# Kernel tuning notes

Measured on AMD Instinct MI355X. Metric: run time of the kernel, lower is better.

Reference implementation:

```python
import math
import jax, jax.numpy as jnp
import numpy as np
from jax import lax

# dimensions
B_, H_, W_, w_ = 2, 28, 28, 7
L_ = H_ * W_
DM, EXPAND = 384, 2
DIN = DM * EXPAND            # 768
DS, DCONV = 16, 4
DTR = math.ceil(DM / 16)     # 24
HG, WG = H_ // w_, W_ // w_
K_ = 4                       # directions: h, v, w7, w7_flip

# ---- MultiScan scan/reverse permutations ----
def scan_h(x):  # [B,L,C] -> [B,C,L]
    return jnp.swapaxes(x, 1, 2)

def scan_v(x):  # 'b (h w) d -> b d (w h)'
    B, L, C = x.shape
    return x.reshape(B, H_, W_, C).transpose(0, 3, 2, 1).reshape(B, C, L)

def scan_w(x, flip):  # local windowed scan, w=7
    B, L, C = x.shape
    x = x.reshape(B, HG, w_, WG, w_, C).transpose(0, 5, 1, 3, 2, 4).reshape(B, C, L)
    return x[:, :, ::-1] if flip else x

def rev_h(x):  # [B,C,L] -> [B,C,L]
    return x

def rev_v(x):  # 'b d (h w) -> b d (w h)'
    B, C, L = x.shape
    return x.reshape(B, C, H_, W_).transpose(0, 1, 3, 2).reshape(B, C, L)

def rev_w(x, flip):
    B, C, L = x.shape
    if flip:
        x = x[:, :, ::-1]
    return x.reshape(B, C, HG, WG, w_, w_).transpose(0, 1, 2, 4, 3, 5).reshape(B, C, L)

# ---- mamba_inner (causal depthwise conv + silu + selective scan) ----
def mamba_inner(xz, conv_w, conv_b, x_proj_w, dt_w, dt_b, A_log, Dp):
    # xz: [B, 2*DIN, L]
    B = xz.shape[0]
    x, z = xz[:, :DIN], xz[:, DIN:]
    xpad = jnp.pad(x, ((0, 0), (0, 0), (DCONV - 1, 0)))  # causal padding
    conv = lax.conv_general_dilated(
        xpad, conv_w[:, None, :], (1,), 'VALID',
        dimension_numbers=('NCH', 'OIH', 'NCH'), feature_group_count=DIN)
    conv = conv + conv_b[None, :, None]
    conv = conv * jax.nn.sigmoid(conv)  # silu
    x_dbl = jnp.einsum('bdl,ed->bel', conv, x_proj_w)  # [B, DTR+2*DS, L]
    dt, Bm, Cm = x_dbl[:, :DTR], x_dbl[:, DTR:DTR + DS], x_dbl[:, DTR + DS:]
    delta = jax.nn.softplus(jnp.einsum('brl,dr->bdl', dt, dt_w) + dt_b[None, :, None])
    A = -jnp.exp(A_log)  # [DIN, DS]
    dA = jnp.exp(jnp.einsum('bdl,dn->lbdn', delta, A))      # [L,B,DIN,DS]
    dBu = jnp.einsum('bdl,bnl,bdl->lbdn', delta, Bm, conv)  # [L,B,DIN,DS]
    Ct = jnp.moveaxis(Cm, -1, 0)                            # [L,B,DS]
    def step(h, inp):
        a, bu, c = inp
        h = a * h + bu
        return h, jnp.einsum('bdn,bn->bd', h, c)
    h0 = jnp.zeros((B, DIN, DS), xz.dtype)
    _, ys = lax.scan(step, h0, (dA, dBu, Ct))  # ys: [L,B,DIN]
    y = jnp.moveaxis(ys, 0, -1) + Dp[:, None] * conv
    return y * (z * jax.nn.sigmoid(z))  # gated with silu(z)

# ---- BiAttn channel gating (shared params across directions) ----
def biattn(x, ln_g, ln_b, gr_w, gr_b, cs_w, cs_b):
    # x: [..., L, DIN]
    mu = x.mean(-1, keepdims=True)
    var = x.var(-1, keepdims=True)
    xn = (x - mu) * lax.rsqrt(var + 1e-5) * ln_g + ln_b
    g = xn.mean(-2, keepdims=True)  # global token
    g = jax.nn.gelu(g @ gr_w.T + gr_b, approximate=False)
    attn = jax.nn.sigmoid(g @ cs_w.T + cs_b)
    return x * attn

def _forward(x, in_proj_w, conv_w, conv_b, x_proj_w, dt_w, dt_b, A_log, Dp,
             ln_g, ln_b, gr_w, gr_b, cs_w, cs_b, out_proj_w):
    xz = x @ in_proj_w.T  # [B,L,2*DIN]
    xs = jnp.stack([scan_h(xz), scan_v(xz), scan_w(xz, False), scan_w(xz, True)])  # [K,B,2DIN,L]
    ys = jax.vmap(mamba_inner)(xs, conv_w, conv_b, x_proj_w, dt_w, dt_b, A_log, Dp)  # [K,B,DIN,L]
    outs = jnp.stack([rev_h(ys[0]), rev_v(ys[1]), rev_w(ys[2], False), rev_w(ys[3], True)])
    outs = jnp.swapaxes(outs, -2, -1)  # [K,B,L,DIN]
    outs = biattn(outs, ln_g, ln_b, gr_w, gr_b, cs_w, cs_b)
    out = outs.sum(0)  # MultiScan merge (search=False)
    return out @ out_proj_w.T  # [B,L,DM]

def setup_inputs() -> dict:
    key = jax.random.key(0)
    ks = jax.random.split(key, 10)
    f = jnp.float32
    return {
        'x': jax.random.normal(ks[0], (B_, L_, DM), f),
        'in_proj_w': jax.random.normal(ks[1], (2 * DIN, DM), f) * 0.02,
        'conv_w': jax.random.normal(ks[2], (K_, DIN, DCONV), f) * 0.2,
        'conv_b': jax.random.normal(ks[3], (K_, DIN), f) * 0.02,
        'x_proj_w': jax.random.normal(ks[4], (K_, DTR + 2 * DS, DIN), f) * 0.02,
        'dt_w': jax.random.normal(ks[5], (K_, DIN, DTR), f) * 0.02,
        'dt_b': jax.random.normal(ks[6], (K_, DIN), f) * 0.02 - 4.0,
        'A_log': jnp.log(jnp.tile(jnp.arange(1, DS + 1, dtype=f)[None, None], (K_, DIN, 1))),
        'Dp': jnp.ones((K_, DIN), f),
        'ln_g': jnp.ones((DIN,), f),
        'ln_b': jnp.zeros((DIN,), f),
        'gr_w': jax.random.normal(ks[7], (DIN // 8, DIN), f) * 0.02,
        'gr_b': jnp.zeros((DIN // 8,), f),
        'cs_w': jax.random.normal(ks[8], (DIN, DIN // 8), f) * 0.02,
        'cs_b': jnp.zeros((DIN,), f),
        'out_proj_w': jax.random.normal(ks[9], (DM, DIN), f) * 0.02,
    }

def reference(x, in_proj_w, conv_w, conv_b, x_proj_w, dt_w, dt_b, A_log, Dp,
              ln_g, ln_b, gr_w, gr_b, cs_w, cs_b, out_proj_w):
    return _forward(x, in_proj_w, conv_w, conv_b, x_proj_w, dt_w, dt_b, A_log, Dp,
                    ln_g, ln_b, gr_w, gr_b, cs_w, cs_b, out_proj_w)
```

## Files before the change

### kernel.cpp

```cpp
#include <hip/hip_runtime.h>
#include <math.h>

#define Bb 2
#define Hh 28
#define Ww 28
#define Ll 784
#define DMm 384
#define DINn 768
#define DSs 16
#define DTRr 24
#define Ee 56
#define Kk 4
#define BL 1568
#define NC 56
#define CH 14

typedef short s8v __attribute__((ext_vector_type(8)));
typedef float f4v __attribute__((ext_vector_type(4)));

__device__ __forceinline__ unsigned short f2bf(float f) {
    unsigned int u = __float_as_uint(f);
    return (unsigned short)((u + 0x7fffu + ((u >> 16) & 1u)) >> 16);
}
__device__ __forceinline__ float bf2f(unsigned short s) {
    return __uint_as_float(((unsigned int)s) << 16);
}

__device__ __forceinline__ int spos(int k, int l) {
    if (k == 0) return l;
    if (k == 1) return (l % 28) * 28 + l / 28;
    if (k == 3) l = 783 - l;
    int j = l % 7;
    int i = (l / 7) % 7;
    int wg = (l / 49) % 4;
    int hg = l / 196;
    return (hg * 7 + i) * 28 + wg * 7 + j;
}


__global__ __launch_bounds__(256) void gemm_mfma(
    const float* __restrict__ A, const float* __restrict__ B, float* __restrict__ Cc,
    int M, int N, int K, int lda, int ldb, int ldc,
    long sA, long sB, long sC, int nsk)
{
    int zz = blockIdx.z;
    int sk = zz % nsk, z = zz / nsk;
    int Kc = K / nsk;
    const float* Ab = A + (long)z * sA + (long)sk * Kc;
    const float* Bp = B + (long)z * sB + (long)sk * Kc;
    float* Cb = Cc + (long)zz * sC;

    __shared__ __align__(16) short Ah[64][40];
    __shared__ __align__(16) short Al[64][40];
    __shared__ __align__(16) short Bh[64][40];
    __shared__ __align__(16) short Bl[64][40];

    int t = threadIdx.x;
    int m0 = blockIdx.y * 64, n0 = blockIdx.x * 64;
    int srow = t >> 2, skq = t & 3;
    int am = m0 + srow;
    int bn = n0 + srow;
    int w = t >> 6, lane = t & 63;
    int wr = (w >> 1) * 32, wc = (w & 1) * 32;
    int lr = lane & 15, lg = lane >> 4;

    f4v acc[2][2] = {};

    int nsteps = Kc / 32;
    float4 a0, a1, b0, b1;
    {
        int koff = skq * 8;
        if (am < M) { a0 = *(const float4*)(Ab + (long)am * lda + koff);
                      a1 = *(const float4*)(Ab + (long)am * lda + koff + 4); }
        else        { a0 = make_float4(0.f,0.f,0.f,0.f); a1 = a0; }
        if (bn < N) { b0 = *(const float4*)(Bp + (long)bn * ldb + koff);
                      b1 = *(const float4*)(Bp + (long)bn * ldb + koff + 4); }
        else        { b0 = make_float4(0.f,0.f,0.f,0.f); b1 = b0; }
    }

    for (int it = 0; it < nsteps; ++it) {
        {
            float va[8] = {a0.x,a0.y,a0.z,a0.w,a1.x,a1.y,a1.z,a1.w};
            float vb[8] = {b0.x,b0.y,b0.z,b0.w,b1.x,b1.y,b1.z,b1.w};
            s8v ah, al2, bh, bl2;
#pragma unroll
            for (int j = 0; j < 8; ++j) {
                unsigned short h = f2bf(va[j]);
                ah[j]  = (short)h;
                al2[j] = (short)f2bf(va[j] - bf2f(h));
                unsigned short g = f2bf(vb[j]);
                bh[j]  = (short)g;
                bl2[j] = (short)f2bf(vb[j] - bf2f(g));
            }
            *(s8v*)&Ah[srow][skq * 8] = ah;
            *(s8v*)&Al[srow][skq * 8] = al2;
            *(s8v*)&Bh[srow][skq * 8] = bh;
            *(s8v*)&Bl[srow][skq * 8] = bl2;
        }
        __syncthreads();

        float4 na0, na1, nb0, nb1;
        if (it + 1 < nsteps) {
            int koff = (it + 1) * 32 + skq * 8;
            if (am < M) { na0 = *(const float4*)(Ab + (long)am * lda + koff);
                          na1 = *(const float4*)(Ab + (long)am * lda + koff + 4); }
            else        { na0 = make_float4(0.f,0.f,0.f,0.f); na1 = na0; }
            if (bn < N) { nb0 = *(const float4*)(Bp + (long)bn * ldb + koff);
                          nb1 = *(const float4*)(Bp + (long)bn * ldb + koff + 4); }
            else        { nb0 = make_float4(0.f,0.f,0.f,0.f); nb1 = nb0; }
        }

        s8v fah[2], fal[2], fbh[2], fbl[2];
#pragma unroll
        for (int rb = 0; rb < 2; ++rb) {
            int r = wr + rb * 16 + lr;
            fah[rb] = *(const s8v*)&Ah[r][lg * 8];
            fal[rb] = *(const s8v*)&Al[r][lg * 8];
        }
#pragma unroll
        for (int cb = 0; cb < 2; ++cb) {
            int c = wc + cb * 16 + lr;
            fbh[cb] = *(const s8v*)&Bh[c][lg * 8];
            fbl[cb] = *(const s8v*)&Bl[c][lg * 8];
        }
#pragma unroll
        for (int rb = 0; rb < 2; ++rb)
#pragma unroll
            for (int cb = 0; cb < 2; ++cb) {
                acc[rb][cb] = __builtin_amdgcn_mfma_f32_16x16x32_bf16(fah[rb], fbh[cb], acc[rb][cb], 0, 0, 0);
                acc[rb][cb] = __builtin_amdgcn_mfma_f32_16x16x32_bf16(fah[rb], fbl[cb], acc[rb][cb], 0, 0, 0);
                acc[rb][cb] = __builtin_amdgcn_mfma_f32_16x16x32_bf16(fal[rb], fbh[cb], acc[rb][cb], 0, 0, 0);
            }
        __syncthreads();
        a0 = na0; a1 = na1; b0 = nb0; b1 = nb1;
    }

#pragma unroll
    for (int rb = 0; rb < 2; ++rb)
#pragma unroll
        for (int cb = 0; cb < 2; ++cb) {
            int n = n0 + wc + cb * 16 + lr;
            if (n >= N) continue;
#pragma unroll
            for (int j = 0; j < 4; ++j) {
                int m = m0 + wr + rb * 16 + lg * 4 + j;
                if (m < M) Cb[(long)m * ldc + n] = acc[rb][cb][j];
            }
        }
}

__global__ __launch_bounds__(256) void reduce_sk(
    const float* __restrict__ part, float* __restrict__ out,
    int M, int Nv, int ldp, int ldo, int nsk, long sSlice, long sOutZ, int nz)
{
    long idx = (long)blockIdx.x * 256 + threadIdx.x;
    long tot = (long)nz * M * Nv;
    if (idx >= tot) return;
    int n = (int)(idx % Nv);
    long r = idx / Nv;
    int m = (int)(r % M);
    int z = (int)(r / M);
    float s = 0.f;
    for (int sk = 0; sk < nsk; ++sk)
        s += part[(long)(z * nsk + sk) * sSlice + (long)m * ldp + n];
    out[(long)z * sOutZ + (long)m * ldo + n] = s;
}

__global__ __launch_bounds__(256) void wsum_kernel(
    const float* __restrict__ outy, const float* __restrict__ attn,
    float* __restrict__ sbuf)
{
    long idx4 = (long)blockIdx.x * 256 + threadIdx.x;
    long tot4 = (long)Bb * Ll * DINn / 4;
    if (idx4 >= tot4) return;
    int d4 = (int)(idx4 % (DINn / 4));
    long bl = idx4 / (DINn / 4);
    int b = (int)(bl / Ll);
    int p = (int)(bl % Ll);
    float4 acc = make_float4(0.f, 0.f, 0.f, 0.f);
#pragma unroll
    for (int k = 0; k < Kk; ++k) {
        int kb = k * 2 + b;
        float4 y = reinterpret_cast<const float4*>(outy + ((long)kb * Ll + p) * DINn)[d4];
        float4 a = reinterpret_cast<const float4*>(attn + (long)kb * DINn)[d4];
        acc.x += y.x * a.x; acc.y += y.y * a.y;
        acc.z += y.z * a.z; acc.w += y.w * a.w;
    }
    reinterpret_cast<float4*>(sbuf)[idx4] = acc;
}

__global__ __launch_bounds__(256) void conv_kernel(
    const float* __restrict__ xz, const float* __restrict__ conv_w,
    const float* __restrict__ conv_b, float* __restrict__ conv,
    const float* __restrict__ dt_w, float* __restrict__ dtw_t)
{
    int l = blockIdx.x;
    int kb = blockIdx.y;
    int k = kb >> 1, b = kb & 1;
    if (kb == 0 && blockIdx.x < 12) {
        int t2 = blockIdx.x * 256 + threadIdx.x;
        int d2 = t2 % DINn, k2 = t2 / DINn;
#pragma unroll
        for (int r = 0; r < DTRr; ++r)
            dtw_t[((long)(k2 * DTRr + r)) * DINn + d2] = dt_w[((long)(k2 * DINn + d2)) * DTRr + r];
    }
    int p[4];
#pragma unroll
    for (int j = 0; j < 4; ++j) {
        int lp = l - 3 + j;
        p[j] = (lp >= 0) ? spos(k, lp) : -1;
    }
    for (int d = threadIdx.x; d < DINn; d += 256) {
        float acc = conv_b[k * DINn + d];
        const float* w = conv_w + (long)(k * DINn + d) * 4;
#pragma unroll
        for (int j = 0; j < 4; ++j) {
            if (p[j] >= 0)
                acc += w[j] * xz[((long)b * Ll + p[j]) * (2 * DINn) + d];
        }
        acc = acc / (1.f + __expf(-acc));
        conv[((long)kb * Ll + l) * DINn + d] = acc;
    }
}

__global__ __launch_bounds__(256) void scan1_kernel(
    const float* __restrict__ conv, const float* __restrict__ part3,
    const float* __restrict__ dtw_t, const float* __restrict__ dt_b,
    const float* __restrict__ Dp,
    float* __restrict__ outy, float* __restrict__ chunkB, float* __restrict__ chunkS,
    float* __restrict__ xdbl)
{
    int d = blockIdx.x * 256 + threadIdx.x;
    int c = blockIdx.y;
    int kb = blockIdx.z;
    int k = kb >> 1, b = kb & 1;

    __shared__ __align__(16) float xrow[CH][Ee];
    {
        int mbase = b * Ll + c * CH;
        for (int u = threadIdx.x; u < CH * Ee; u += 256) {
            int i = u / Ee, j = u % Ee;
            long base = ((long)(k * 8) * BL + mbase + i) * 56 + j;
            float s = 0.f;
#pragma unroll
            for (int sk = 0; sk < 8; ++sk)
                s += part3[base + (long)sk * BL * 56];
            xrow[i][j] = s;
            if (blockIdx.x == 0)
                xdbl[((long)kb * Ll + c * CH) * Ee + u] = s;
        }
    }
    __syncthreads();

    float dtw[DTRr];
#pragma unroll
    for (int r = 0; r < DTRr; ++r) dtw[r] = dtw_t[((long)(k * DTRr + r)) * DINn + d];
    float dtb = dt_b[k * DINn + d];
    float Dv = Dp[k * DINn + d];
    float h[DSs];
#pragma unroll
    for (int n = 0; n < DSs; ++n) h[n] = 0.f;

    const float* cl = conv + ((long)kb * Ll + c * CH) * DINn + d;
    float sumde = 0.f;
    for (int i = 0; i < CH; ++i) {
        const float4* xr = reinterpret_cast<const float4*>(&xrow[i][0]);
        float xlin = dtb;
#pragma unroll
        for (int g = 0; g < 6; ++g) {
            float4 q = xr[g];
            xlin += dtw[4*g] * q.x + dtw[4*g+1] * q.y + dtw[4*g+2] * q.z + dtw[4*g+3] * q.w;
        }
        float tE = __expf(xlin);
        float E = __builtin_amdgcn_rcpf(1.f + tE);
        float de = (xlin > 15.f) ? xlin : -__logf(E);
        float cv = cl[(long)i * DINn];
        sumde += de;
        float dexc = de * cv;
        float dAn = E;
        float y = Dv * cv;
#pragma unroll
        for (int g = 0; g < 4; ++g) {
            float4 Bq = xr[6 + g];
            float4 Cq = xr[10 + g];
            h[4*g+0] = dAn * h[4*g+0] + dexc * Bq.x; y += h[4*g+0] * Cq.x; dAn *= E;
            h[4*g+1] = dAn * h[4*g+1] + dexc * Bq.y; y += h[4*g+1] * Cq.y; dAn *= E;
            h[4*g+2] = dAn * h[4*g+2] + dexc * Bq.z; y += h[4*g+2] * Cq.z; dAn *= E;
            h[4*g+3] = dAn * h[4*g+3] + dexc * Bq.w; y += h[4*g+3] * Cq.w; dAn *= E;
        }
        int l = c * CH + i;
        int p = spos(k, l);
        outy[((long)kb * Ll + p) * DINn + d] = y;
    }
    long o = (long)(kb * NC + c);
    chunkS[o * DINn + d] = sumde;
#pragma unroll
    for (int n = 0; n < DSs; ++n)
        chunkB[(o * DSs + n) * DINn + d] = h[n];
}

__global__ __launch_bounds__(256) void scanfix_kernel(
    const float* __restrict__ chunkS, float* chunkB)
{
    int u = blockIdx.x * 256 + threadIdx.x;
    int d = u % DINn;
    int rest = u / DINn;
    int n = rest & 15;
    int kb = rest >> 4;
    float np1 = (float)(n + 1);
    float h = 0.f;
#pragma unroll
    for (int c = 0; c < NC; ++c) {
        long o = (long)(kb * NC + c);
        float S = chunkS[o * DINn + d];
        float a = __expf(-np1 * S);
        long idx = (o * DSs + n) * DINn + d;
        float bv = chunkB[idx];
        chunkB[idx] = h;
        h = a * h + bv;
    }
}

__global__ __launch_bounds__(768) void scan3_kernel(
    const float* __restrict__ xdbl, const float* __restrict__ dtw_t,
    const float* __restrict__ dt_b, const float* __restrict__ hin,
    const float* __restrict__ xz, float* __restrict__ outy,
    float* __restrict__ gpart)
{
    int d = threadIdx.x;
    int c = blockIdx.x;
    int kb = blockIdx.y;
    int k = kb >> 1, b = kb & 1;

    __shared__ __align__(16) float xrow[CH][Ee];
    {
        const float* src = xdbl + ((long)kb * Ll + c * CH) * Ee;
        for (int u = threadIdx.x; u < CH * Ee; u += 768)
            xrow[u / Ee][u % Ee] = src[u];
    }
    __syncthreads();

    float dtw[DTRr];
#pragma unroll
    for (int r = 0; r < DTRr; ++r) dtw[r] = dtw_t[((long)(k * DTRr + r)) * DINn + d];
    float dtb = dt_b[k * DINn + d];
    long o = (long)(kb * NC + c);
    float hc[DSs];
#pragma unroll
    for (int n = 0; n < DSs; ++n) hc[n] = hin[(o * DSs + n) * DINn + d];

    float v[CH];
    for (int i = 0; i < CH; ++i) {
        const float4* xr = reinterpret_cast<const float4*>(&xrow[i][0]);
        float xlin = dtb;
#pragma unroll
        for (int g = 0; g < 6; ++g) {
            float4 q = xr[g];
            xlin += dtw[4*g] * q.x + dtw[4*g+1] * q.y + dtw[4*g+2] * q.z + dtw[4*g+3] * q.w;
        }
        float E = __builtin_amdgcn_rcpf(1.f + __expf(xlin));
        int l = c * CH + i;
        int p = spos(k, l);
        long oy = ((long)kb * Ll + p) * DINn + d;
        float y = outy[oy];
        const float4* Cq4 = reinterpret_cast<const float4*>(&xrow[i][40]);
        float dAn = E;
#pragma unroll
        for (int g = 0; g < 4; ++g) {
            float4 Cq = Cq4[g];
            hc[4*g+0] *= dAn; y += hc[4*g+0] * Cq.x; dAn *= E;
            hc[4*g+1] *= dAn; y += hc[4*g+1] * Cq.y; dAn *= E;
            hc[4*g+2] *= dAn; y += hc[4*g+2] * Cq.z; dAn *= E;
            hc[4*g+3] *= dAn; y += hc[4*g+3] * Cq.w; dAn *= E;
        }
        float zv = xz[((long)b * Ll + p) * (2 * DINn) + DINn + d];
        y *= zv / (1.f + __expf(-zv));
        outy[oy] = y;
        v[i] = y;
    }

    int w = threadIdx.x >> 6, lane = threadIdx.x & 63;
    __shared__ float ps[12][CH], pss[12][CH];
    __shared__ float smu[CH], srs[CH];
#pragma unroll
    for (int i = 0; i < CH; ++i) {
        float s = v[i], ss = v[i] * v[i];
#pragma unroll
        for (int of = 32; of > 0; of >>= 1) {
            s += __shfl_down(s, of);
            ss += __shfl_down(ss, of);
        }
        if (lane == 0) { ps[w][i] = s; pss[w][i] = ss; }
    }
    __syncthreads();
    if (threadIdx.x < CH) {
        float s = 0.f, ss = 0.f;
#pragma unroll
        for (int w2 = 0; w2 < 12; ++w2) { s += ps[w2][threadIdx.x]; ss += pss[w2][threadIdx.x]; }
        float m = s / DINn;
        float var = ss / DINn - m * m;
        smu[threadIdx.x] = m;
        srs[threadIdx.x] = rsqrtf(var + 1e-5f);
    }
    __syncthreads();
    float acc = 0.f;
#pragma unroll
    for (int i = 0; i < CH; ++i) acc += (v[i] - smu[i]) * srs[i];
    gpart[(o) * DINn + d] = acc;
}

__global__ __launch_bounds__(768) void attn_kernel(
    const float* __restrict__ gpart, const float* __restrict__ ln_g,
    const float* __restrict__ ln_b, const float* __restrict__ gr_w,
    const float* __restrict__ gr_b, const float* __restrict__ cs_w,
    const float* __restrict__ cs_b, float* __restrict__ attn)
{
    __shared__ float gs[DINn];
    __shared__ float hs[96];
    int kb = blockIdx.x;
    int t = threadIdx.x;
    int w = t >> 6, lane = t & 63;
    {
        float s = 0.f;
#pragma unroll
        for (int c = 0; c < NC; ++c)
            s += gpart[((long)kb * NC + c) * DINn + t];
        gs[t] = ln_g[t] * (s / (float)Ll) + ln_b[t];
    }
    __syncthreads();
#pragma unroll
    for (int rr = 0; rr < 8; ++rr) {
        int r = w * 8 + rr;
        const float* wrow = gr_w + (long)r * DINn;
        float s = 0.f;
#pragma unroll
        for (int e = 0; e < 12; ++e) s += wrow[lane + 64 * e] * gs[lane + 64 * e];
#pragma unroll
        for (int o = 32; o > 0; o >>= 1) s += __shfl_down(s, o);
        if (lane == 0) {
            float a = s + gr_b[r];
            hs[r] = 0.5f * a * (1.f + erff(a * 0.70710678118654752f));
        }
    }
    __syncthreads();
    {
        float a = cs_b[t];
        const float4* wr = reinterpret_cast<const float4*>(cs_w + (long)t * 96);
#pragma unroll
        for (int e = 0; e < 24; ++e) {
            float4 q = wr[e];
            a += q.x * hs[4*e] + q.y * hs[4*e+1] + q.z * hs[4*e+2] + q.w * hs[4*e+3];
        }
        attn[kb * DINn + t] = 1.f / (1.f + __expf(-a));
    }
}

extern "C" void kernel_launch(void* const* d_in, const int* in_sizes, int n_in,
                              void* d_out, int out_size, void* d_ws, size_t ws_size,
                              hipStream_t stream) {
    const float* x         = (const float*)d_in[0];
    const float* in_proj_w = (const float*)d_in[1];
    const float* conv_w    = (const float*)d_in[2];
    const float* conv_b    = (const float*)d_in[3];
    const float* x_proj_w  = (const float*)d_in[4];
    const float* dt_w      = (const float*)d_in[5];
    const float* dt_b      = (const float*)d_in[6];
    const float* Dp        = (const float*)d_in[8];
    const float* ln_g      = (const float*)d_in[9];
    const float* ln_b      = (const float*)d_in[10];
    const float* gr_w      = (const float*)d_in[11];
    const float* gr_b      = (const float*)d_in[12];
    const float* cs_w      = (const float*)d_in[13];
    const float* cs_b      = (const float*)d_in[14];
    const float* out_proj_w= (const float*)d_in[15];
    float* out = (float*)d_out;

    float* ws     = (float*)d_ws;
    float* xz     = ws;
    float* conv   = xz    + (long)Bb * Ll * 2 * DINn;
    float* outy   = conv  + (long)Kk * BL * DINn;
    float* gpart  = outy  + (long)Kk * BL * DINn;
    float* attn   = gpart + (long)Kk * Bb * NC * DINn;
    float* dtw_t  = attn  + 2 * Kk * DINn;
    float* xdbl   = dtw_t + (long)Kk * DTRr * DINn;
    float* chunkB = xdbl  + (long)Kk * BL * Ee;
    float* chunkS = chunkB + (long)Kk * Bb * NC * DSs * DINn;
    float* part3  = chunkS + (long)Kk * Bb * NC * DINn;
    float* sbuf   = part3 + (long)32 * BL * 56;
    float* part10 = part3;

    gemm_mfma<<<dim3(1536 / 64, (BL + 63) / 64, 1), 256, 0, stream>>>(
        x, in_proj_w, xz, BL, 2 * DINn, DMm, DMm, DMm, 2 * DINn, 0, 0, 0, 1);

    conv_kernel<<<dim3(Ll, Kk * Bb), 256, 0, stream>>>(
        xz, conv_w, conv_b, conv, dt_w, dtw_t);

    gemm_mfma<<<dim3(1, (BL + 63) / 64, Kk * 8), 256, 0, stream>>>(
        conv, x_proj_w, part3, BL, Ee, DINn, DINn, DINn, 56,
        (long)BL * DINn, (long)Ee * DINn, (long)BL * 56, 8);

    scan1_kernel<<<dim3(DINn / 256, NC, Kk * Bb), 256, 0, stream>>>(
        conv, part3, dtw_t, dt_b, Dp, outy, chunkB, chunkS, xdbl);

    scanfix_kernel<<<dim3((Kk * Bb * DSs * DINn) / 256), 256, 0, stream>>>(
        chunkS, chunkB);

    scan3_kernel<<<dim3(NC, Kk * Bb), 768, 0, stream>>>(
        xdbl, dtw_t, dt_b, chunkB, xz, outy, gpart);

    attn_kernel<<<dim3(Kk * Bb), 768, 0, stream>>>(
        gpart, ln_g, ln_b, gr_w, gr_b, cs_w, cs_b, attn);

    wsum_kernel<<<dim3((Bb * Ll * DINn / 4 + 255) / 256), 256, 0, stream>>>(
        outy, attn, sbuf);

    gemm_mfma<<<dim3(DMm / 64, (BL + 63) / 64, 4), 256, 0, stream>>>(
        sbuf, out_proj_w, part10, BL, DMm, DINn, DINn, DINn, DMm,
        0, 0, (long)BL * DMm, 4);
    reduce_sk<<<dim3((BL * DMm + 255) / 256), 256, 0, stream>>>(
        part10, out, BL, DMm, DMm, DMm, 4, (long)BL * DMm, 0, 1);
}
```

Baseline: 258.4 us.

## Fuse attention into scan3 via last-block counter, atomic split-K output, wider scan1 blocks

Removes the separate attn_kernel by having the last-arriving scan3 block for each (k,b) compute the gated attention, using a global atomic counter with threadfences. The counter is reset in conv_kernel. The out_proj split-K GEMM now accumulates into the output with atomicAdd, after wsum zeroes it, which drops the reduce_sk kernel. scan1 is relaunched as one 768-thread block per chunk so each block covers all channels. Together these cut two kernel launches, but float atomics make summation order nondeterministic and the last-block pattern adds serialized tail work.

```diff
diff --git a/kernel.cpp b/kernel.cpp
--- a/kernel.cpp
+++ b/kernel.cpp
@@ -41,7 +41,7 @@
 __global__ __launch_bounds__(256) void gemm_mfma(
     const float* __restrict__ A, const float* __restrict__ B, float* __restrict__ Cc,
     int M, int N, int K, int lda, int ldb, int ldc,
-    long sA, long sB, long sC, int nsk)
+    long sA, long sB, long sC, int nsk, int atomic_out)
 {
     int zz = blockIdx.z;
     int sk = zz % nsk, z = zz / nsk;
@@ -144,33 +144,21 @@
 #pragma unroll
             for (int j = 0; j < 4; ++j) {
                 int m = m0 + wr + rb * 16 + lg * 4 + j;
-                if (m < M) Cb[(long)m * ldc + n] = acc[rb][cb][j];
+                if (m < M) {
+                    if (atomic_out) atomicAdd(&Cb[(long)m * ldc + n], acc[rb][cb][j]);
+                    else            Cb[(long)m * ldc + n] = acc[rb][cb][j];
+                }
             }
         }
-}
-
-__global__ __launch_bounds__(256) void reduce_sk(
-    const float* __restrict__ part, float* __restrict__ out,
-    int M, int Nv, int ldp, int ldo, int nsk, long sSlice, long sOutZ, int nz)
-{
-    long idx = (long)blockIdx.x * 256 + threadIdx.x;
-    long tot = (long)nz * M * Nv;
-    if (idx >= tot) return;
-    int n = (int)(idx % Nv);
-    long r = idx / Nv;
-    int m = (int)(r % M);
-    int z = (int)(r / M);
-    float s = 0.f;
-    for (int sk = 0; sk < nsk; ++sk)
-        s += part[(long)(z * nsk + sk) * sSlice + (long)m * ldp + n];
-    out[(long)z * sOutZ + (long)m * ldo + n] = s;
 }
 
 __global__ __launch_bounds__(256) void wsum_kernel(
     const float* __restrict__ outy, const float* __restrict__ attn,
-    float* __restrict__ sbuf)
+    float* __restrict__ sbuf, float* __restrict__ out)
 {
     long idx4 = (long)blockIdx.x * 256 + threadIdx.x;
+    if (idx4 < (long)BL * DMm / 4)
+        reinterpret_cast<float4*>(out)[idx4] = make_float4(0.f, 0.f, 0.f, 0.f);
     long tot4 = (long)Bb * Ll * DINn / 4;
     if (idx4 >= tot4) return;
     int d4 = (int)(idx4 % (DINn / 4));
@@ -192,11 +180,13 @@
 __global__ __launch_bounds__(256) void conv_kernel(
     const float* __restrict__ xz, const float* __restrict__ conv_w,
     const float* __restrict__ conv_b, float* __restrict__ conv,
-    const float* __restrict__ dt_w, float* __restrict__ dtw_t)
+    const float* __restrict__ dt_w, float* __restrict__ dtw_t,
+    int* __restrict__ ctr)
 {
     int l = blockIdx.x;
     int kb = blockIdx.y;
     int k = kb >> 1, b = kb & 1;
+    if (kb == 0 && blockIdx.x == 0 && threadIdx.x < 8) ctr[threadIdx.x] = 0;
     if (kb == 0 && blockIdx.x < 12) {
         int t2 = blockIdx.x * 256 + threadIdx.x;
         int d2 = t2 % DINn, k2 = t2 / DINn;
@@ -223,22 +213,22 @@
     }
 }
 
-__global__ __launch_bounds__(256) void scan1_kernel(
+__global__ __launch_bounds__(768) void scan1_kernel(
     const float* __restrict__ conv, const float* __restrict__ part3,
     const float* __restrict__ dtw_t, const float* __restrict__ dt_b,
     const float* __restrict__ Dp,
     float* __restrict__ outy, float* __restrict__ chunkB, float* __restrict__ chunkS,
     float* __restrict__ xdbl)
 {
-    int d = blockIdx.x * 256 + threadIdx.x;
-    int c = blockIdx.y;
-    int kb = blockIdx.z;
+    int d = threadIdx.x;
+    int c = blockIdx.x;
+    int kb = blockIdx.y;
     int k = kb >> 1, b = kb & 1;
 
     __shared__ __align__(16) float xrow[CH][Ee];
     {
         int mbase = b * Ll + c * CH;
-        for (int u = threadIdx.x; u < CH * Ee; u += 256) {
+        for (int u = threadIdx.x; u < CH * Ee; u += 768) {
             int i = u / Ee, j = u % Ee;
             long base = ((long)(k * 8) * BL + mbase + i) * 56 + j;
             float s = 0.f;
@@ -246,8 +236,7 @@
             for (int sk = 0; sk < 8; ++sk)
                 s += part3[base + (long)sk * BL * 56];
             xrow[i][j] = s;
-            if (blockIdx.x == 0)
-                xdbl[((long)kb * Ll + c * CH) * Ee + u] = s;
+            xdbl[((long)kb * Ll + c * CH) * Ee + u] = s;
         }
     }
     __syncthreads();
@@ -325,7 +314,11 @@
     const float* __restrict__ xdbl, const float* __restrict__ dtw_t,
     const float* __restrict__ dt_b, const float* __restrict__ hin,
     const float* __restrict__ xz, float* __restrict__ outy,
-    float* __restrict__ gpart)
+    float* __restrict__ gpart,
+    const float* __restrict__ ln_g, const float* __restrict__ ln_b,
+    const float* __restrict__ gr_w, const float* __restrict__ gr_b,
+    const float* __restrict__ cs_w, const float* __restrict__ cs_b,
+    float* __restrict__ attn, int* __restrict__ ctr)
 {
     int d = threadIdx.x;
     int c = blockIdx.x;
@@ -407,24 +400,22 @@
 #pragma unroll
     for (int i = 0; i < CH; ++i) acc += (v[i] - smu[i]) * srs[i];
     gpart[(o) * DINn + d] = acc;
-}
-
-__global__ __launch_bounds__(768) void attn_kernel(
-    const float* __restrict__ gpart, const float* __restrict__ ln_g,
-    const float* __restrict__ ln_b, const float* __restrict__ gr_w,
-    const float* __restrict__ gr_b, const float* __restrict__ cs_w,
-    const float* __restrict__ cs_b, float* __restrict__ attn)
-{
+
+    __threadfence();
+    __shared__ int lastf;
+    if (threadIdx.x == 0) lastf = (atomicAdd(&ctr[kb], 1) == NC - 1) ? 1 : 0;
+    __syncthreads();
+    if (!lastf) return;
+    __threadfence();
+
     __shared__ float gs[DINn];
     __shared__ float hs[96];
-    int kb = blockIdx.x;
     int t = threadIdx.x;
-    int w = t >> 6, lane = t & 63;
     {
         float s = 0.f;
 #pragma unroll
-        for (int c = 0; c < NC; ++c)
-            s += gpart[((long)kb * NC + c) * DINn + t];
+        for (int cc = 0; cc < NC; ++cc)
+            s += gpart[((long)kb * NC + cc) * DINn + t];
         gs[t] = ln_g[t] * (s / (float)Ll) + ln_b[t];
     }
     __syncthreads();
@@ -436,7 +427,7 @@
 #pragma unroll
         for (int e = 0; e < 12; ++e) s += wrow[lane + 64 * e] * gs[lane + 64 * e];
 #pragma unroll
-        for (int o = 32; o > 0; o >>= 1) s += __shfl_down(s, o);
+        for (int of = 32; of > 0; of >>= 1) s += __shfl_down(s, of);
         if (lane == 0) {
             float a = s + gr_b[r];
             hs[r] = 0.5f * a * (1.f + erff(a * 0.70710678118654752f));
@@ -487,36 +478,32 @@
     float* chunkS = chunkB + (long)Kk * Bb * NC * DSs * DINn;
     float* part3  = chunkS + (long)Kk * Bb * NC * DINn;
     float* sbuf   = part3 + (long)32 * BL * 56;
-    float* part10 = part3;
+    int*   ctr    = (int*)(sbuf + (long)Bb * Ll * DINn);
 
     gemm_mfma<<<dim3(1536 / 64, (BL + 63) / 64, 1), 256, 0, stream>>>(
-        x, in_proj_w, xz, BL, 2 * DINn, DMm, DMm, DMm, 2 * DINn, 0, 0, 0, 1);
+        x, in_proj_w, xz, BL, 2 * DINn, DMm, DMm, DMm, 2 * DINn, 0, 0, 0, 1, 0);
 
     conv_kernel<<<dim3(Ll, Kk * Bb), 256, 0, stream>>>(
-        xz, conv_w, conv_b, conv, dt_w, dtw_t);
+        xz, conv_w, conv_b, conv, dt_w, dtw_t, ctr);
 
     gemm_mfma<<<dim3(1, (BL + 63) / 64, Kk * 8), 256, 0, stream>>>(
         conv, x_proj_w, part3, BL, Ee, DINn, DINn, DINn, 56,
-        (long)BL * DINn, (long)Ee * DINn, (long)BL * 56, 8);
-
-    scan1_kernel<<<dim3(DINn / 256, NC, Kk * Bb), 256, 0, stream>>>(
+        (long)BL * DINn, (long)Ee * DINn, (long)BL * 56, 8, 0);
+
+    scan1_kernel<<<dim3(NC, Kk * Bb), 768, 0, stream>>>(
         conv, part3, dtw_t, dt_b, Dp, outy, chunkB, chunkS, xdbl);
 
     scanfix_kernel<<<dim3((Kk * Bb * DSs * DINn) / 256), 256, 0, stream>>>(
         chunkS, chunkB);
 
     scan3_kernel<<<dim3(NC, Kk * Bb), 768, 0, stream>>>(
-        xdbl, dtw_t, dt_b, chunkB, xz, outy, gpart);
-
-    attn_kernel<<<dim3(Kk * Bb), 768, 0, stream>>>(
-        gpart, ln_g, ln_b, gr_w, gr_b, cs_w, cs_b, attn);
+        xdbl, dtw_t, dt_b, chunkB, xz, outy, gpart,
+        ln_g, ln_b, gr_w, gr_b, cs_w, cs_b, attn, ctr);
 
     wsum_kernel<<<dim3((Bb * Ll * DINn / 4 + 255) / 256), 256, 0, stream>>>(
-        outy, attn, sbuf);
+        outy, attn, sbuf, out);
 
     gemm_mfma<<<dim3(DMm / 64, (BL + 63) / 64, 4), 256, 0, stream>>>(
-        sbuf, out_proj_w, part10, BL, DMm, DINn, DINn, DINn, DMm,
-        0, 0, (long)BL * DMm, 4);
-    reduce_sk<<<dim3((BL * DMm + 255) / 256), 256, 0, stream>>>(
-        part10, out, BL, DMm, DMm, DMm, 4, (long)BL * DMm, 0, 1);
-}
+        sbuf, out_proj_w, out, BL, DMm, DINn, DINn, DINn, DMm,
+        0, 0, 0, 4, 1);
+}
```

Result: slower. 346.7 us (+34.2%).
